# Optimization experiments

Measured on AMD Instinct MI355X. Metric: run time of the kernel, lower is better.

## Reference

```python
import jax, jax.numpy as jnp
import numpy as np

N = 100000   # nodes
E = 1600000  # edges per edge list (avg degree 16)
G = 512      # graphs in batch
D = 128      # hidden dim
BN_EPS = 1e-5


def setup_inputs() -> dict:
    key = jax.random.key(0)
    kit = iter(jax.random.split(key, 100))
    def nrm(shape, s=0.05):
        return jax.random.normal(next(kit), shape, dtype=jnp.float32) * s
    d = {}
    d['x_type'] = nrm((N, 3), 1.0)
    d['first'] = nrm((N, 13), 1.0)
    d['second'] = nrm((N, 13), 1.0)
    d['edge_attr'] = nrm((N, 4), 1.0)
    d['dist'] = jax.random.uniform(next(kit), (N, 1), dtype=jnp.float32)
    # encoder / fusion MLP blocks: Linear-BN-ReLU-Linear-BN-ReLU
    for pre, ind in (('te', 3), ('na', 26), ('ee', 5), ('m0', 3 * D)):
        d[pre + '_W1'] = nrm((ind, D)); d[pre + '_b1'] = jnp.zeros((D,), jnp.float32)
        d[pre + '_g1'] = jnp.ones((D,), jnp.float32); d[pre + '_be1'] = jnp.zeros((D,), jnp.float32)
        d[pre + '_W2'] = nrm((D, D)); d[pre + '_b2'] = jnp.zeros((D,), jnp.float32)
        d[pre + '_g2'] = jnp.ones((D,), jnp.float32); d[pre + '_be2'] = jnp.zeros((D,), jnp.float32)
    # 24 GINConv inner MLPs, stacked: layer L, conv k -> index 4*L+k (k: 1_l,2_l,1_g,2_g)
    d['gW1'] = nrm((24, D, D)); d['gb1'] = jnp.zeros((24, D), jnp.float32)
    d['gg1'] = jnp.ones((24, D), jnp.float32); d['gbe1'] = jnp.zeros((24, D), jnp.float32)
    d['gW2'] = nrm((24, D, D)); d['gb2'] = jnp.zeros((24, D), jnp.float32)
    d['gg2'] = jnp.ones((24, D), jnp.float32); d['gbe2'] = jnp.zeros((24, D), jnp.float32)
    d['geps'] = jnp.zeros((24,), jnp.float32)
    # 6 per-layer fusion MLPs (4*dim -> dim), stacked
    d['mW1'] = nrm((6, 4 * D, D)); d['mb1'] = jnp.zeros((6, D), jnp.float32)
    d['mg1'] = jnp.ones((6, D), jnp.float32); d['mbe1'] = jnp.zeros((6, D), jnp.float32)
    d['mW2'] = nrm((6, D, D)); d['mb2'] = jnp.zeros((6, D), jnp.float32)
    d['mg2'] = jnp.ones((6, D), jnp.float32); d['mbe2'] = jnp.zeros((6, D), jnp.float32)
    # Set2Set LSTM (input 2D, hidden D), torch gate order i,f,g,o
    d['Wih'] = nrm((4 * D, 2 * D)); d['Whh'] = nrm((4 * D, D))
    d['bih'] = jnp.zeros((4 * D,), jnp.float32); d['bhh'] = jnp.zeros((4 * D,), jnp.float32)
    d['fc1_W'] = nrm((2 * D, D)); d['fc1_b'] = jnp.zeros((D,), jnp.float32)
    d['fc4_W'] = nrm((D, 12)); d['fc4_b'] = jnp.zeros((12,), jnp.float32)
    for nm in ('ei_1l', 'ei_2l', 'ei_1g', 'ei_2g'):
        d[nm] = jax.random.randint(next(kit), (2, E), 0, N)
    d['batch'] = jnp.sort(jax.random.randint(next(kit), (N,), 0, G))
    return d


def _bn(h, g, b):
    # BatchNorm1d training-mode forward: biased batch stats
    m = h.mean(0)
    v = ((h - m) ** 2).mean(0)
    return g * (h - m) * jax.lax.rsqrt(v + BN_EPS) + b


def _block(h, W1, b1, g1, be1, W2, b2, g2, be2):
    h = jax.nn.relu(_bn(h @ W1 + b1, g1, be1))
    return jax.nn.relu(_bn(h @ W2 + b2, g2, be2))


def _forward(x_type, first, second, edge_attr, dist,
             te_W1, te_b1, te_g1, te_be1, te_W2, te_b2, te_g2, te_be2,
             na_W1, na_b1, na_g1, na_be1, na_W2, na_b2, na_g2, na_be2,
             ee_W1, ee_b1, ee_g1, ee_be1, ee_W2, ee_b2, ee_g2, ee_be2,
             m0_W1, m0_b1, m0_g1, m0_be1, m0_W2, m0_b2, m0_g2, m0_be2,
             gW1, gb1, gg1, gbe1, gW2, gb2, gg2, gbe2, geps,
             mW1, mb1, mg1, mbe1, mW2, mb2, mg2, mbe2,
             Wih, Whh, bih, bhh, fc1_W, fc1_b, fc4_W, fc4_b,
             ei_1l, ei_2l, ei_1g, ei_2g, batch):
    nl = _block(x_type, te_W1, te_b1, te_g1, te_be1, te_W2, te_b2, te_g2, te_be2)
    na = _block(jnp.concatenate([first, second], -1),
                na_W1, na_b1, na_g1, na_be1, na_W2, na_b2, na_g2, na_be2)
    ea = _block(jnp.concatenate([edge_attr, dist], -1),
                ee_W1, ee_b1, ee_g1, ee_be1, ee_W2, ee_b2, ee_g2, ee_be2)
    x = _block(jnp.concatenate([nl, na, ea], -1),
               m0_W1, m0_b1, m0_g1, m0_be1, m0_W2, m0_b2, m0_g2, m0_be2)

    def gin(h, ei, i):
        # GINConv: nn((1+eps)*x_i + sum_{j in N(i)} x_j); messages src=ei[0] -> dst=ei[1]
        agg = jnp.zeros_like(h).at[ei[1]].add(h[ei[0]])
        z = (1.0 + geps[i]) * h + agg
        return jax.nn.relu(_block(z, gW1[i], gb1[i], gg1[i], gbe1[i],
                                  gW2[i], gb2[i], gg2[i], gbe2[i]))

    for L in range(6):
        x1 = gin(x, ei_1l, 4 * L + 0)
        x2 = gin(x, ei_2l, 4 * L + 1)
        x3 = gin(x, ei_1g, 4 * L + 2)
        x4 = gin(x, ei_2g, 4 * L + 3)
        x = _block(jnp.concatenate([x1, x3, x2, x4], -1),
                   mW1[L], mb1[L], mg1[L], mbe1[L], mW2[L], mb2[L], mg2[L], mbe2[L])

    # Set2Set, 6 processing steps
    q_star = jnp.zeros((G, 2 * D), x.dtype)
    h = jnp.zeros((G, D), x.dtype)
    c = jnp.zeros((G, D), x.dtype)
    for _ in range(6):
        z = q_star @ Wih.T + h @ Whh.T + bih + bhh
        i_, f_, g_, o_ = jnp.split(z, 4, axis=1)
        c = jax.nn.sigmoid(f_) * c + jax.nn.sigmoid(i_) * jnp.tanh(g_)
        h = jax.nn.sigmoid(o_) * jnp.tanh(c)
        e = jnp.sum(x * h[batch], axis=-1)                     # [N]
        emax = jax.ops.segment_max(e, batch, num_segments=G)
        w = jnp.exp(e - emax[batch])
        den = jax.ops.segment_sum(w, batch, num_segments=G)
        a = w / den[batch]                                     # per-graph softmax
        r = jax.ops.segment_sum(a[:, None] * x, batch, num_segments=G)
        q_star = jnp.concatenate([h, r], axis=1)

    out = jax.nn.relu(q_star @ fc1_W + fc1_b) @ fc4_W + fc4_b  # [G, 12]
    return out


def reference(x_type, first, second, edge_attr, dist,
              te_W1, te_b1, te_g1, te_be1, te_W2, te_b2, te_g2, te_be2,
              na_W1, na_b1, na_g1, na_be1, na_W2, na_b2, na_g2, na_be2,
              ee_W1, ee_b1, ee_g1, ee_be1, ee_W2, ee_b2, ee_g2, ee_be2,
              m0_W1, m0_b1, m0_g1, m0_be1, m0_W2, m0_b2, m0_g2, m0_be2,
              gW1, gb1, gg1, gbe1, gW2, gb2, gg2, gbe2, geps,
              mW1, mb1, mg1, mbe1, mW2, mb2, mg2, mbe2,
              Wih, Whh, bih, bhh, fc1_W, fc1_b, fc4_W, fc4_b,
              ei_1l, ei_2l, ei_1g, ei_2g, batch):
    return _forward(x_type, first, second, edge_attr, dist,
                    te_W1, te_b1, te_g1, te_be1, te_W2, te_b2, te_g2, te_be2,
                    na_W1, na_b1, na_g1, na_be1, na_W2, na_b2, na_g2, na_be2,
                    ee_W1, ee_b1, ee_g1, ee_be1, ee_W2, ee_b2, ee_g2, ee_be2,
                    m0_W1, m0_b1, m0_g1, m0_be1, m0_W2, m0_b2, m0_g2, m0_be2,
                    gW1, gb1, gg1, gbe1, gW2, gb2, gg2, gbe2, geps,
                    mW1, mb1, mg1, mbe1, mW2, mb2, mg2, mbe2,
                    Wih, Whh, bih, bhh, fc1_W, fc1_b, fc4_W, fc4_b,
                    ei_1l, ei_2l, ei_1g, ei_2g, batch)
```

## Files before the change

kernel.cpp:

```cpp
#include <hip/hip_runtime.h>
#include <math.h>


#define DEV_INLINE __device__ __forceinline__
typedef unsigned short u16;

union F16U { _Float16 h; u16 u; };
DEV_INLINE float h2f(u16 v){ F16U t; t.u = v; return (float)t.h; }
DEV_INLINE u16 f2h(float f){ F16U t; t.h = (_Float16)f; return t.u; }
DEV_INLINE float bf2f(u16 h){ return __uint_as_float(((unsigned)h)<<16); }
DEV_INLINE u16 f2bf(float f){
  unsigned u = __float_as_uint(f);
  unsigned r = (u + 0x7FFFu + ((u>>16)&1u)) >> 16;
  return (u16)r;
}
DEV_INLINE float sigmoidf_(float x){ return 1.0f/(1.0f+expf(-x)); }
struct __align__(4) us2 { u16 x, y; };
struct __align__(8) us4 { u16 x, y, z, w; };

typedef __attribute__((ext_vector_type(8))) short s8v;
typedef __attribute__((ext_vector_type(4))) float f4v;

DEV_INLINE void bnsplit1(float f, u16& hb, u16& lb){
  hb = f2bf(f); lb = f2bf(f - bf2f(hb));
}

__global__ void zero_k(float* __restrict__ p, int n){
  int i = blockIdx.x*256 + threadIdx.x;
  if (i < n) p[i] = 0.f;
}

__global__ __launch_bounds__(256) void split_transpose(
  const float* __restrict__ src, u16* __restrict__ dh, u16* __restrict__ dl,
  int K, int count)
{
  int tot = count*K*128;
  for (int i = blockIdx.x*256 + threadIdx.x; i < tot; i += gridDim.x*256){
    int k = i % K;
    int n = (i / K) & 127;
    int c = i / (K*128);
    float w = src[(size_t)c*K*128 + (size_t)k*128 + n];
    u16 hi = f2bf(w);
    u16 lo = f2bf(w - bf2f(hi));
    dh[i] = hi; dl[i] = lo;
  }
}

__global__ void count_deg(const int* __restrict__ dst, int* __restrict__ cnt, int E){
  int e = blockIdx.x*256 + threadIdx.x;
  if (e < E) atomicAdd(&cnt[dst[e]], 1);
}

__global__ void scan_excl(const int* __restrict__ cnt, int* __restrict__ offs, int N){
  const int* c = cnt + (size_t)blockIdx.x * N;
  int* o = offs + (size_t)blockIdx.x * (N+1);
  __shared__ int ps[1024];
  int t = threadIdx.x;
  int chunk = (N + 1023) >> 10;
  int lo = t*chunk, hi = min(lo+chunk, N);
  int s = 0;
  for (int i=lo;i<hi;++i) s += c[i];
  ps[t] = s; __syncthreads();
  for (int d=1; d<1024; d<<=1){
    int v = (t>=d) ? ps[t-d] : 0;
    __syncthreads();
    ps[t] += v;
    __syncthreads();
  }
  int pre = (t==0) ? 0 : ps[t-1];
  for (int i=lo;i<hi;++i){ o[i]=pre; pre += c[i]; }
  if (t==1023) o[N] = ps[1023];
}

__global__ void fill_csr(const int* __restrict__ src, const int* __restrict__ dst,
                         const int* __restrict__ offs, int* __restrict__ cur,
                         int* __restrict__ out, int E){
  int e = blockIdx.x*256 + threadIdx.x;
  if (e >= E) return;
  int d = dst[e];
  int pos = offs[d] + atomicAdd(&cur[d], 1);
  out[pos] = src[e];
}

__global__ void sort_csr(const int* __restrict__ offs, int* __restrict__ srcs, int N){
  int i = blockIdx.x*256 + threadIdx.x;
  if (i >= N) return;
  int lo = offs[i], hi = offs[i+1];
  for (int a = lo+1; a < hi; ++a){
    int v = srcs[a];
    int b = a-1;
    while (b >= lo && srcs[b] > v){ srcs[b+1] = srcs[b]; --b; }
    srcs[b+1] = v;
  }
}

__global__ void graph_offsets(const int* __restrict__ batch, int* __restrict__ goff, int N, int G){
  int g = blockIdx.x*blockDim.x + threadIdx.x;
  if (g > G) return;
  int lo=0, hi=N;
  while (lo<hi){ int mid=(lo+hi)>>1; if (batch[mid] < g) lo=mid+1; else hi=mid; }
  goff[g]=lo;
}

__global__ __launch_bounds__(256) void stats_reduce1(
  const float* __restrict__ pstats, int PB, float* __restrict__ out2, int nb)
{
  int c = threadIdx.x, grp = blockIdx.x, bank = blockIdx.y;
  int chunk = (nb + 31) >> 5;
  int b0 = grp*chunk, b1 = min(b0+chunk, nb);
  const float* base = pstats + (size_t)bank*PB*256;
  float s = 0.f;
  for (int b=b0; b<b1; ++b) s += base[(size_t)b*256 + c];
  out2[((size_t)bank*32 + grp)*256 + c] = s;
}
__global__ __launch_bounds__(256) void bnfin2(
  const float* __restrict__ out2, const float* __restrict__ g,
  const float* __restrict__ be, float* __restrict__ Sb, float invN)
{
  __shared__ float tot[256];
  int t = threadIdx.x, bank = blockIdx.x;
  const float* src = out2 + (size_t)bank*32*256;
  float s = 0.f;
  #pragma unroll
  for (int j=0;j<32;++j) s += src[j*256 + t];
  tot[t] = s; __syncthreads();
  if (t < 128){
    float m = tot[t]*invN;
    float v = tot[128+t]*invN - m*m;
    float sc = g[bank*128 + t]*rsqrtf(v + 1e-5f);
    Sb[bank*256 + t] = sc;
    Sb[bank*256 + 128 + t] = be[bank*128 + t] - m*sc;
  }
}

#define GEMM_KS_BODY_F(A_, S_, WHp_, WLp_, Kel_)                              \
  {                                                                           \
    float4 sa0, sa1, sb0, sb1;                                                \
    if (S_){                                                                  \
      sa0 = *(const float4*)(S_ + koff);                                      \
      sa1 = *(const float4*)(S_ + koff + 4);                                  \
      sb0 = *(const float4*)(S_ + 128 + koff);                                \
      sb1 = *(const float4*)(S_ + 128 + koff + 4);                            \
    }                                                                         \
    s8v xh0, xl0, xh1, xl1;                                                   \
    _Pragma("unroll")                                                         \
    for (int mt=0; mt<2; ++mt){                                               \
      int row = wrow0 + mt*16 + m16;                                          \
      s8v xr = (row < N) ? *(const s8v*)(A_ + (size_t)row*128 + koff)         \
                         : (s8v){0,0,0,0,0,0,0,0};                            \
      float f0 = h2f((u16)xr[0]), f1 = h2f((u16)xr[1]);                       \
      float f2 = h2f((u16)xr[2]), f3 = h2f((u16)xr[3]);                       \
      float f4 = h2f((u16)xr[4]), f5 = h2f((u16)xr[5]);                       \
      float f6 = h2f((u16)xr[6]), f7 = h2f((u16)xr[7]);                       \
      if (S_){                                                                \
        f0 = fmaxf(fmaf(f0, sa0.x, sb0.x), 0.f);                              \
        f1 = fmaxf(fmaf(f1, sa0.y, sb0.y), 0.f);                              \
        f2 = fmaxf(fmaf(f2, sa0.z, sb0.z), 0.f);                              \
        f3 = fmaxf(fmaf(f3, sa0.w, sb0.w), 0.f);                              \
        f4 = fmaxf(fmaf(f4, sa1.x, sb1.x), 0.f);                              \
        f5 = fmaxf(fmaf(f5, sa1.y, sb1.y), 0.f);                              \
        f6 = fmaxf(fmaf(f6, sa1.z, sb1.z), 0.f);                              \
        f7 = fmaxf(fmaf(f7, sa1.w, sb1.w), 0.f);                              \
      }                                                                       \
      s8v h, l; u16 hb, lb;                                                   \
      bnsplit1(f0,hb,lb); h[0]=(short)hb; l[0]=(short)lb;                     \
      bnsplit1(f1,hb,lb); h[1]=(short)hb; l[1]=(short)lb;                     \
      bnsplit1(f2,hb,lb); h[2]=(short)hb; l[2]=(short)lb;                     \
      bnsplit1(f3,hb,lb); h[3]=(short)hb; l[3]=(short)lb;                     \
      bnsplit1(f4,hb,lb); h[4]=(short)hb; l[4]=(short)lb;                     \
      bnsplit1(f5,hb,lb); h[5]=(short)hb; l[5]=(short)lb;                     \
      bnsplit1(f6,hb,lb); h[6]=(short)hb; l[6]=(short)lb;                     \
      bnsplit1(f7,hb,lb); h[7]=(short)hb; l[7]=(short)lb;                     \
      if (mt==0){ xh0=h; xl0=l; } else { xh1=h; xl1=l; }                      \
    }                                                                         \
    _Pragma("unroll")                                                         \
    for (int nh=0; nh<2; ++nh){                                               \
      _Pragma("unroll")                                                       \
      for (int n4=0;n4<4;++n4){                                               \
        int n = (nh*4+n4)*16 + m16;                                           \
        size_t wa = (size_t)n*Kel_ + koff;                                    \
        s8v wh = *(const s8v*)(WHp_ + wa);                                    \
        s8v wl = *(const s8v*)(WLp_ + wa);                                    \
        acc[0][nh*4+n4] = __builtin_amdgcn_mfma_f32_16x16x32_bf16(wh, xh0, acc[0][nh*4+n4], 0,0,0); \
        acc[0][nh*4+n4] = __builtin_amdgcn_mfma_f32_16x16x32_bf16(wl, xh0, acc[0][nh*4+n4], 0,0,0); \
        acc[0][nh*4+n4] = __builtin_amdgcn_mfma_f32_16x16x32_bf16(wh, xl0, acc[0][nh*4+n4], 0,0,0); \
        acc[1][nh*4+n4] = __builtin_amdgcn_mfma_f32_16x16x32_bf16(wh, xh1, acc[1][nh*4+n4], 0,0,0); \
        acc[1][nh*4+n4] = __builtin_amdgcn_mfma_f32_16x16x32_bf16(wl, xh1, acc[1][nh*4+n4], 0,0,0); \
        acc[1][nh*4+n4] = __builtin_amdgcn_mfma_f32_16x16x32_bf16(wh, xl1, acc[1][nh*4+n4], 0,0,0); \
      }                                                                       \
    }                                                                         \
  }

#define GEMM_EPILOGUE_F(C_, bias_, pslot_)                                    \
  {                                                                           \
    _Pragma("unroll")                                                         \
    for (int nt=0;nt<8;++nt){                                                 \
      int n0 = nt*16 + kg*4;                                                  \
      float4 b4 = *(const float4*)(bias_ + n0);                               \
      float s1a=0.f,s1b=0.f,s1c=0.f,s1d=0.f;                                  \
      float s2a=0.f,s2b=0.f,s2c=0.f,s2d=0.f;                                  \
      _Pragma("unroll")                                                       \
      for (int mt=0;mt<2;++mt){                                               \
        int row = wrow0 + mt*16 + m16;                                        \
        us4 o;                                                                \
        o.x = f2h(acc[mt][nt][0] + b4.x);                                     \
        o.y = f2h(acc[mt][nt][1] + b4.y);                                     \
        o.z = f2h(acc[mt][nt][2] + b4.z);                                     \
        o.w = f2h(acc[mt][nt][3] + b4.w);                                     \
        *(us4*)(&cst[wid][mt][m16*136 + n0]) = o;                             \
        if (row < N){                                                         \
          float r0=h2f(o.x), r1=h2f(o.y), r2=h2f(o.z), r3=h2f(o.w);           \
          s1a+=r0; s1b+=r1; s1c+=r2; s1d+=r3;                                 \
          s2a+=r0*r0; s2b+=r1*r1; s2c+=r2*r2; s2d+=r3*r3;                     \
        }                                                                     \
      }                                                                       \
      _Pragma("unroll")                                                       \
      for (int off=1; off<16; off<<=1){                                       \
        s1a += __shfl_xor(s1a, off, 64); s1b += __shfl_xor(s1b, off, 64);     \
        s1c += __shfl_xor(s1c, off, 64); s1d += __shfl_xor(s1d, off, 64);     \
        s2a += __shfl_xor(s2a, off, 64); s2b += __shfl_xor(s2b, off, 64);     \
        s2c += __shfl_xor(s2c, off, 64); s2d += __shfl_xor(s2d, off, 64);     \
      }                                                                       \
      if (m16 == 0){                                                          \
        pw[wid][n0+0] = s1a; pw[wid][n0+1] = s1b;                             \
        pw[wid][n0+2] = s1c; pw[wid][n0+3] = s1d;                             \
        pw[wid][128+n0+0] = s2a; pw[wid][128+n0+1] = s2b;                     \
        pw[wid][128+n0+2] = s2c; pw[wid][128+n0+3] = s2d;                     \
      }                                                                       \
    }                                                                         \
    __syncthreads();                                                          \
    if (t < 256){                                                             \
      float tot = ((pw[0][t] + pw[1][t]) + pw[2][t]) + pw[3][t];              \
      (pslot_)[t] = tot;                                                      \
    }                                                                         \
    _Pragma("unroll")                                                         \
    for (int mt=0;mt<2;++mt){                                                 \
      _Pragma("unroll")                                                       \
      for (int it=0; it<4; ++it){                                             \
        int idx = it*64 + lane;                                               \
        int r = idx >> 4;                                                     \
        int c8 = (idx & 15) * 8;                                              \
        int row = wrow0 + mt*16 + r;                                          \
        if (row < N){                                                         \
          s8v v = *(const s8v*)(&cst[wid][mt][r*136 + c8]);                   \
          *(s8v*)(C_ + (size_t)row*128 + c8) = v;                             \
        }                                                                     \
      }                                                                       \
    }                                                                         \
  }

#define GEMM_KS_BODY_S(A_, S_, WHp_, WLp_, Kel_)                              \
  {                                                                           \
    float4 sa0, sa1, sb0, sb1;                                                \
    if (S_){                                                                  \
      sa0 = *(const float4*)(S_ + koff);                                      \
      sa1 = *(const float4*)(S_ + koff + 4);                                  \
      sb0 = *(const float4*)(S_ + 128 + koff);                                \
      sb1 = *(const float4*)(S_ + 128 + koff + 4);                            \
    }                                                                         \
    s8v xh0, xl0, xh1, xl1;                                                   \
    _Pragma("unroll")                                                         \
    for (int mt=0; mt<2; ++mt){                                               \
      int row = wrow0 + mt*16 + m16;                                          \
      s8v xr = (row < N) ? *(const s8v*)(A_ + (size_t)row*128 + koff)         \
                         : (s8v){0,0,0,0,0,0,0,0};                            \
      float f0 = h2f((u16)xr[0]), f1 = h2f((u16)xr[1]);                       \
      float f2 = h2f((u16)xr[2]), f3 = h2f((u16)xr[3]);                       \
      float f4 = h2f((u16)xr[4]), f5 = h2f((u16)xr[5]);                       \
      float f6 = h2f((u16)xr[6]), f7 = h2f((u16)xr[7]);                       \
      if (S_){                                                                \
        f0 = fmaxf(fmaf(f0, sa0.x, sb0.x), 0.f);                              \
        f1 = fmaxf(fmaf(f1, sa0.y, sb0.y), 0.f);                              \
        f2 = fmaxf(fmaf(f2, sa0.z, sb0.z), 0.f);                              \
        f3 = fmaxf(fmaf(f3, sa0.w, sb0.w), 0.f);                              \
        f4 = fmaxf(fmaf(f4, sa1.x, sb1.x), 0.f);                              \
        f5 = fmaxf(fmaf(f5, sa1.y, sb1.y), 0.f);                              \
        f6 = fmaxf(fmaf(f6, sa1.z, sb1.z), 0.f);                              \
        f7 = fmaxf(fmaf(f7, sa1.w, sb1.w), 0.f);                              \
      }                                                                       \
      s8v h, l; u16 hb, lb;                                                   \
      bnsplit1(f0,hb,lb); h[0]=(short)hb; l[0]=(short)lb;                     \
      bnsplit1(f1,hb,lb); h[1]=(short)hb; l[1]=(short)lb;                     \
      bnsplit1(f2,hb,lb); h[2]=(short)hb; l[2]=(short)lb;                     \
      bnsplit1(f3,hb,lb); h[3]=(short)hb; l[3]=(short)lb;                     \
      bnsplit1(f4,hb,lb); h[4]=(short)hb; l[4]=(short)lb;                     \
      bnsplit1(f5,hb,lb); h[5]=(short)hb; l[5]=(short)lb;                     \
      bnsplit1(f6,hb,lb); h[6]=(short)hb; l[6]=(short)lb;                     \
      bnsplit1(f7,hb,lb); h[7]=(short)hb; l[7]=(short)lb;                     \
      if (mt==0){ xh0=h; xl0=l; } else { xh1=h; xl1=l; }                      \
    }                                                                         \
    _Pragma("unroll")                                                         \
    for (int nt=0; nt<4; ++nt){                                               \
      int n = colbase + nt*16 + m16;                                          \
      size_t wa = (size_t)n*Kel_ + koff;                                      \
      s8v wh = *(const s8v*)(WHp_ + wa);                                      \
      s8v wl = *(const s8v*)(WLp_ + wa);                                      \
      acc[0][nt] = __builtin_amdgcn_mfma_f32_16x16x32_bf16(wh, xh0, acc[0][nt], 0,0,0); \
      acc[0][nt] = __builtin_amdgcn_mfma_f32_16x16x32_bf16(wl, xh0, acc[0][nt], 0,0,0); \
      acc[0][nt] = __builtin_amdgcn_mfma_f32_16x16x32_bf16(wh, xl0, acc[0][nt], 0,0,0); \
      acc[1][nt] = __builtin_amdgcn_mfma_f32_16x16x32_bf16(wh, xh1, acc[1][nt], 0,0,0); \
      acc[1][nt] = __builtin_amdgcn_mfma_f32_16x16x32_bf16(wl, xh1, acc[1][nt], 0,0,0); \
      acc[1][nt] = __builtin_amdgcn_mfma_f32_16x16x32_bf16(wh, xl1, acc[1][nt], 0,0,0); \
    }                                                                         \
  }

#define GEMM_EPILOGUE_S(C_, bias_, pslot_)                                    \
  {                                                                           \
    _Pragma("unroll")                                                         \
    for (int nt=0;nt<4;++nt){                                                 \
      int lc0 = nt*16 + kg*4;                                                 \
      int n0 = colbase + lc0;                                                 \
      float4 b4 = *(const float4*)(bias_ + n0);                               \
      float s1a=0.f,s1b=0.f,s1c=0.f,s1d=0.f;                                  \
      float s2a=0.f,s2b=0.f,s2c=0.f,s2d=0.f;                                  \
      _Pragma("unroll")                                                       \
      for (int mt=0;mt<2;++mt){                                               \
        int row = wrow0 + mt*16 + m16;                                        \
        us4 o;                                                                \
        o.x = f2h(acc[mt][nt][0] + b4.x);                                     \
        o.y = f2h(acc[mt][nt][1] + b4.y);                                     \
        o.z = f2h(acc[mt][nt][2] + b4.z);                                     \
        o.w = f2h(acc[mt][nt][3] + b4.w);                                     \
        *(us4*)(&cst[wid][mt][m16*72 + lc0]) = o;                             \
        if (row < N){                                                         \
          float r0=h2f(o.x), r1=h2f(o.y), r2=h2f(o.z), r3=h2f(o.w);           \
          s1a+=r0; s1b+=r1; s1c+=r2; s1d+=r3;                                 \
          s2a+=r0*r0; s2b+=r1*r1; s2c+=r2*r2; s2d+=r3*r3;                     \
        }                                                                     \
      }                                                                       \
      _Pragma("unroll")                                                       \
      for (int off=1; off<16; off<<=1){                                       \
        s1a += __shfl_xor(s1a, off, 64); s1b += __shfl_xor(s1b, off, 64);     \
        s1c += __shfl_xor(s1c, off, 64); s1d += __shfl_xor(s1d, off, 64);     \
        s2a += __shfl_xor(s2a, off, 64); s2b += __shfl_xor(s2b, off, 64);     \
        s2c += __shfl_xor(s2c, off, 64); s2d += __shfl_xor(s2d, off, 64);     \
      }                                                                       \
      if (m16 == 0){                                                          \
        pw[wid][lc0+0] = s1a; pw[wid][lc0+1] = s1b;                           \
        pw[wid][lc0+2] = s1c; pw[wid][lc0+3] = s1d;                           \
        pw[wid][64+lc0+0] = s2a; pw[wid][64+lc0+1] = s2b;                     \
        pw[wid][64+lc0+2] = s2c; pw[wid][64+lc0+3] = s2d;                     \
      }                                                                       \
    }                                                                         \
    __syncthreads();                                                          \
    if (t < 128){                                                             \
      int lc = t & 63, part = t >> 6;                                         \
      int li = part*64 + lc;                                                  \
      float tot = ((pw[0][li] + pw[1][li]) + pw[2][li]) + pw[3][li];          \
      (pslot_)[part*128 + colbase + lc] = tot;                                \
    }                                                                         \
    _Pragma("unroll")                                                         \
    for (int mt=0;mt<2;++mt){                                                 \
      _Pragma("unroll")                                                       \
      for (int it=0; it<2; ++it){                                             \
        int idx = it*64 + lane;                                               \
        int r = idx >> 3;                                                     \
        int c8 = (idx & 7) * 8;                                               \
        int row = wrow0 + mt*16 + r;                                          \
        if (row < N){                                                         \
          s8v v = *(const s8v*)(&cst[wid][mt][r*72 + c8]);                    \
          *(s8v*)(C_ + (size_t)row*128 + colbase + c8) = v;                   \
        }                                                                     \
      }                                                                       \
    }                                                                         \
  }

__global__ __launch_bounds__(256, 3) void gemm_rs_full(
  const u16* __restrict__ A0, const u16* __restrict__ A1,
  const u16* __restrict__ A2, const u16* __restrict__ A3,
  const float* __restrict__ S0, const float* __restrict__ S1,
  const float* __restrict__ S2, const float* __restrict__ S3,
  const u16* __restrict__ wt_hi, const u16* __restrict__ wt_lo,
  const float* __restrict__ bias,
  u16* __restrict__ C, float* __restrict__ pstats,
  int N, int npart)
{
  __shared__ u16 cst[4][2][16*136];
  __shared__ float pw[4][256];
  const int t = threadIdx.x;
  const int lane = t & 63;
  const int wid = t >> 6;
  const int m16 = lane & 15;
  const int kg = lane >> 4;
  const int wrow0 = blockIdx.x*128 + wid*32;
  const int K = npart << 7;

  f4v acc[2][8];
  #pragma unroll
  for (int i=0;i<2;++i)
    #pragma unroll
    for (int j=0;j<8;++j) acc[i][j] = (f4v){0.f,0.f,0.f,0.f};

  for (int part=0; part<npart; ++part){
    const u16* A = (part==0)?A0:(part==1)?A1:(part==2)?A2:A3;
    const float* S = (part==0)?S0:(part==1)?S1:(part==2)?S2:S3;
    const u16* WHp = wt_hi + part*128;
    const u16* WLp = wt_lo + part*128;
    #pragma unroll
    for (int ks=0; ks<4; ++ks){
      int koff = ks*32 + kg*8;
      GEMM_KS_BODY_F(A, S, WHp, WLp, K)
    }
  }
  GEMM_EPILOGUE_F(C, bias, (pstats + (size_t)blockIdx.x*256))
}

__global__ __launch_bounds__(256, 3) void gemm_rs_split(
  const u16* __restrict__ A0, const u16* __restrict__ A1,
  const u16* __restrict__ A2, const u16* __restrict__ A3,
  const float* __restrict__ S0, const float* __restrict__ S1,
  const float* __restrict__ S2, const float* __restrict__ S3,
  const u16* __restrict__ wt_hi, const u16* __restrict__ wt_lo,
  const float* __restrict__ bias,
  u16* __restrict__ C, float* __restrict__ pstats,
  int N, int npart)
{
  __shared__ u16 cst[4][2][16*72];
  __shared__ float pw[4][128];
  const int t = threadIdx.x;
  const int lane = t & 63;
  const int wid = t >> 6;
  const int m16 = lane & 15;
  const int kg = lane >> 4;
  const int wrow0 = blockIdx.x*128 + wid*32;
  const int colbase = blockIdx.y*64;
  const int K = npart << 7;

  f4v acc[2][4];
  #pragma unroll
  for (int i=0;i<2;++i)
    #pragma unroll
    for (int j=0;j<4;++j) acc[i][j] = (f4v){0.f,0.f,0.f,0.f};

  for (int part=0; part<npart; ++part){
    const u16* A = (part==0)?A0:(part==1)?A1:(part==2)?A2:A3;
    const float* S = (part==0)?S0:(part==1)?S1:(part==2)?S2:S3;
    const u16* WHp = wt_hi + part*128;
    const u16* WLp = wt_lo + part*128;
    #pragma unroll
    for (int ks=0; ks<4; ++ks){
      int koff = ks*32 + kg*8;
      GEMM_KS_BODY_S(A, S, WHp, WLp, K)
    }
  }
  GEMM_EPILOGUE_S(C, bias, (pstats + (size_t)blockIdx.x*256))
}

__global__ __launch_bounds__(256, 3) void gemm_gin(
  u16* __restrict__ Z0, u16* __restrict__ Z1,
  u16* __restrict__ Z2, u16* __restrict__ Z3,
  const float* __restrict__ Sbase,
  const u16* __restrict__ wt_hi, const u16* __restrict__ wt_lo,
  const float* __restrict__ bias,
  float* __restrict__ pstats, int PB,
  int N)
{
  __shared__ u16 cst[4][2][16*136];
  __shared__ float pw[4][256];
  const int t = threadIdx.x;
  const int lane = t & 63;
  const int wid = t >> 6;
  const int m16 = lane & 15;
  const int kg = lane >> 4;
  const int wrow0 = blockIdx.x*128 + wid*32;
  const int kb = blockIdx.y;

  u16* Zc = (kb==0)?Z0:(kb==1)?Z1:(kb==2)?Z2:Z3;
  const float* S = Sbase ? (Sbase + (size_t)kb*256) : nullptr;
  const u16* WHp = wt_hi + (size_t)kb*16384;
  const u16* WLp = wt_lo + (size_t)kb*16384;
  const float* biasp = bias + (size_t)kb*128;
  float* pslot = pstats + ((size_t)kb*PB + blockIdx.x)*256;

  f4v acc[2][8];
  #pragma unroll
  for (int i=0;i<2;++i)
    #pragma unroll
    for (int j=0;j<8;++j) acc[i][j] = (f4v){0.f,0.f,0.f,0.f};

  {
    const u16* A = Zc;
    #pragma unroll
    for (int ks=0; ks<4; ++ks){
      int koff = ks*32 + kg*8;
      GEMM_KS_BODY_F(A, S, WHp, WLp, 128)
    }
  }
  GEMM_EPILOGUE_F(Zc, biasp, pslot)
}

__global__ __launch_bounds__(256) void gemm_enc(
  const float* __restrict__ X0, int w0, const float* __restrict__ X1, int w1,
  const float* __restrict__ W, const float* __restrict__ bias,
  u16* __restrict__ C, float* __restrict__ pstats, int N)
{
  __shared__ float Ws[26*128];
  __shared__ float red[256];
  int K = w0 + w1;
  int t = threadIdx.x;
  for (int i=t;i<K*128;i+=256) Ws[i] = W[i];
  __syncthreads();
  int c = t & 127, rh = t >> 7;
  float b = bias[c];
  float s1=0.f, s2=0.f;
  for (int r0 = blockIdx.x*2; r0 < N; r0 += gridDim.x*2){
    int r = r0 + rh;
    if (r < N){
      float acc = b;
      for (int k=0;k<w0;++k) acc = fmaf(X0[(size_t)r*w0+k], Ws[k*128+c], acc);
      for (int k=0;k<w1;++k) acc = fmaf(X1[(size_t)r*w1+k], Ws[(w0+k)*128+c], acc);
      u16 o = f2h(acc);
      C[(size_t)r*128+c] = o;
      float rv = h2f(o);
      s1 += rv; s2 += rv*rv;
    }
  }
  red[t] = s1; __syncthreads();
  float t1 = (t < 128) ? (red[t] + red[t+128]) : 0.f;
  __syncthreads();
  red[t] = s2; __syncthreads();
  float t2 = (t < 128) ? (red[t] + red[t+128]) : 0.f;
  if (t < 128){
    pstats[(size_t)blockIdx.x*256 + t] = t1;
    pstats[(size_t)blockIdx.x*256 + 128 + t] = t2;
  }
}

__global__ __launch_bounds__(256) void aggregate4(
  const u16* __restrict__ X, const float* __restrict__ S,
  const int* __restrict__ srcs4, const int* __restrict__ offs4,
  int E, int Np1, const float* __restrict__ geps, int gi0,
  u16* __restrict__ Z0, u16* __restrict__ Z1,
  u16* __restrict__ Z2, u16* __restrict__ Z3, int N)
{
  int kb = blockIdx.y;
  const int* srcs = srcs4 + (size_t)kb*E;
  const int* offs = offs4 + (size_t)kb*Np1;
  u16* Z = (kb==0)?Z0:(kb==1)?Z1:(kb==2)?Z2:Z3;
  int i = blockIdx.x*4 + (threadIdx.x>>6);
  int ln = threadIdx.x & 63;
  int c = ln*2;
  if (i >= N) return;
  float sca = S[c], sha = S[128+c];
  float scb = S[c+1], shb = S[128+c+1];
  float eps1 = 1.0f + geps[gi0 + kb];
  us2 x0 = *(const us2*)(X + (size_t)i*128 + c);
  float acca = eps1 * fmaxf(fmaf(h2f(x0.x), sca, sha), 0.f);
  float accb = eps1 * fmaxf(fmaf(h2f(x0.y), scb, shb), 0.f);
  int e0 = offs[i], e1 = offs[i+1];
  int e = e0;
  for (; e+8 <= e1; e += 8){
    int s0 = srcs[e],   s1 = srcs[e+1], s2 = srcs[e+2], s3 = srcs[e+3];
    int s4 = srcs[e+4], s5 = srcs[e+5], s6 = srcs[e+6], s7 = srcs[e+7];
    us2 v0 = *(const us2*)(X + (size_t)s0*128 + c);
    us2 v1 = *(const us2*)(X + (size_t)s1*128 + c);
    us2 v2 = *(const us2*)(X + (size_t)s2*128 + c);
    us2 v3 = *(const us2*)(X + (size_t)s3*128 + c);
    us2 v4 = *(const us2*)(X + (size_t)s4*128 + c);
    us2 v5 = *(const us2*)(X + (size_t)s5*128 + c);
    us2 v6 = *(const us2*)(X + (size_t)s6*128 + c);
    us2 v7 = *(const us2*)(X + (size_t)s7*128 + c);
    acca += fmaxf(fmaf(h2f(v0.x), sca, sha), 0.f);
    accb += fmaxf(fmaf(h2f(v0.y), scb, shb), 0.f);
    acca += fmaxf(fmaf(h2f(v1.x), sca, sha), 0.f);
    accb += fmaxf(fmaf(h2f(v1.y), scb, shb), 0.f);
    acca += fmaxf(fmaf(h2f(v2.x), sca, sha), 0.f);
    accb += fmaxf(fmaf(h2f(v2.y), scb, shb), 0.f);
    acca += fmaxf(fmaf(h2f(v3.x), sca, sha), 0.f);
    accb += fmaxf(fmaf(h2f(v3.y), scb, shb), 0.f);
    acca += fmaxf(fmaf(h2f(v4.x), sca, sha), 0.f);
    accb += fmaxf(fmaf(h2f(v4.y), scb, shb), 0.f);
    acca += fmaxf(fmaf(h2f(v5.x), sca, sha), 0.f);
    accb += fmaxf(fmaf(h2f(v5.y), scb, shb), 0.f);
    acca += fmaxf(fmaf(h2f(v6.x), sca, sha), 0.f);
    accb += fmaxf(fmaf(h2f(v6.y), scb, shb), 0.f);
    acca += fmaxf(fmaf(h2f(v7.x), sca, sha), 0.f);
    accb += fmaxf(fmaf(h2f(v7.y), scb, shb), 0.f);
  }
  for (; e+4 <= e1; e += 4){
    int s0 = srcs[e], s1 = srcs[e+1], s2 = srcs[e+2], s3 = srcs[e+3];
    us2 v0 = *(const us2*)(X + (size_t)s0*128 + c);
    us2 v1 = *(const us2*)(X + (size_t)s1*128 + c);
    us2 v2 = *(const us2*)(X + (size_t)s2*128 + c);
    us2 v3 = *(const us2*)(X + (size_t)s3*128 + c);
    acca += fmaxf(fmaf(h2f(v0.x), sca, sha), 0.f);
    accb += fmaxf(fmaf(h2f(v0.y), scb, shb), 0.f);
    acca += fmaxf(fmaf(h2f(v1.x), sca, sha), 0.f);
    accb += fmaxf(fmaf(h2f(v1.y), scb, shb), 0.f);
    acca += fmaxf(fmaf(h2f(v2.x), sca, sha), 0.f);
    accb += fmaxf(fmaf(h2f(v2.y), scb, shb), 0.f);
    acca += fmaxf(fmaf(h2f(v3.x), sca, sha), 0.f);
    accb += fmaxf(fmaf(h2f(v3.y), scb, shb), 0.f);
  }
  for (; e < e1; ++e){
    int s = srcs[e];
    us2 xv = *(const us2*)(X + (size_t)s*128 + c);
    acca += fmaxf(fmaf(h2f(xv.x), sca, sha), 0.f);
    accb += fmaxf(fmaf(h2f(xv.y), scb, shb), 0.f);
  }
  us2 o; o.x = f2h(acca); o.y = f2h(accb);
  *(us2*)(Z + (size_t)i*128 + c) = o;
}

__global__ __launch_bounds__(256) void lstm_step(
  float* __restrict__ q_star, float* __restrict__ h, float* __restrict__ cst,
  const float* __restrict__ Wih, const float* __restrict__ Whh,
  const float* __restrict__ bih, const float* __restrict__ bhh, int G)
{
  __shared__ float q[256], hh[128], z[512];
  int t = threadIdx.x;
  for (int g = blockIdx.x; g < G; g += gridDim.x){
    q[t] = q_star[(size_t)g*256 + t];
    if (t < 128) hh[t] = h[(size_t)g*128 + t];
    __syncthreads();
    #pragma unroll
    for (int p=0;p<2;++p){
      int j = t + 256*p;
      float acc = bih[j] + bhh[j];
      const float* wi = Wih + (size_t)j*256;
      const float* wh = Whh + (size_t)j*128;
      for (int k=0;k<256;++k) acc = fmaf(q[k], wi[k], acc);
      for (int k=0;k<128;++k) acc = fmaf(hh[k], wh[k], acc);
      z[j] = acc;
    }
    __syncthreads();
    if (t < 128){
      float i_ = z[t], f_ = z[128+t], g_ = z[256+t], o_ = z[384+t];
      float cc = sigmoidf_(f_)*cst[(size_t)g*128+t] + sigmoidf_(i_)*tanhf(g_);
      float hn = sigmoidf_(o_)*tanhf(cc);
      cst[(size_t)g*128+t] = cc;
      h[(size_t)g*128+t]  = hn;
      q_star[(size_t)g*256+t] = hn;
    }
    __syncthreads();
  }
}

__global__ __launch_bounds__(256) void dot_h_hf(
  const u16* __restrict__ X, const float* __restrict__ S,
  const float* __restrict__ h, const int* __restrict__ batch,
  float* __restrict__ e, int N)
{
  int wv = threadIdx.x >> 6, ln = threadIdx.x & 63;
  int i = blockIdx.x*4 + wv;
  if (i >= N) return;
  int g = batch[i];
  int c = ln*2;
  us2 x2 = *(const us2*)(X + (size_t)i*128 + c);
  float2 h2 = *(const float2*)(h + (size_t)g*128 + c);
  float xa = fmaxf(fmaf(h2f(x2.x), S[c],   S[128+c]),   0.f);
  float xb = fmaxf(fmaf(h2f(x2.y), S[c+1], S[128+c+1]), 0.f);
  float p = xa*h2.x + xb*h2.y;
  #pragma unroll
  for (int off=32; off; off>>=1) p += __shfl_down(p, off, 64);
  if (ln==0) e[i] = p;
}

__global__ __launch_bounds__(256) void seg_reduce(
  const float* __restrict__ e, const int* __restrict__ goff,
  float* __restrict__ emax, float* __restrict__ invden, int G)
{
  int g = blockIdx.x;
  int lo = goff[g], hi = goff[g+1];
  int t = threadIdx.x;
  __shared__ float red[256];
  float m = -3.4e38f;
  for (int i=lo+t; i<hi; i+=256) m = fmaxf(m, e[i]);
  red[t] = m; __syncthreads();
  for (int d=128; d; d>>=1){ if (t<d) red[t] = fmaxf(red[t], red[t+d]); __syncthreads(); }
  m = red[0]; __syncthreads();
  float s = 0.f;
  for (int i=lo+t; i<hi; i+=256) s += expf(e[i]-m);
  red[t] = s; __syncthreads();
  for (int d=128; d; d>>=1){ if (t<d) red[t] += red[t+d]; __syncthreads(); }
  if (t==0){
    emax[g] = m;
    invden[g] = (hi>lo && red[0]>0.f) ? 1.f/red[0] : 0.f;
  }
}

__global__ __launch_bounds__(128) void r_kernel_hf(
  const u16* __restrict__ X, const float* __restrict__ S,
  const float* __restrict__ e, const int* __restrict__ goff,
  const float* __restrict__ emax, const float* __restrict__ invden,
  float* __restrict__ q_star, int G)
{
  int g = blockIdx.x, c = threadIdx.x;
  int lo = goff[g], hi = goff[g+1];
  float m = emax[g], inv = invden[g];
  float sc = S[c], sh = S[128+c];
  float r = 0.f;
  for (int i=lo; i<hi; ++i){
    float w = expf(e[i]-m);
    r = fmaf(w, fmaxf(fmaf(h2f(X[(size_t)i*128+c]), sc, sh), 0.f), r);
  }
  q_star[(size_t)g*256 + 128 + c] = r*inv;
}

__global__ __launch_bounds__(128) void final_k(
  const float* __restrict__ q_star, const float* __restrict__ fc1W,
  const float* __restrict__ fc1b, const float* __restrict__ fc4W,
  const float* __restrict__ fc4b, float* __restrict__ out, int G)
{
  __shared__ float q[256];
  __shared__ float h1[128];
  int g = blockIdx.x, t = threadIdx.x;
  q[t]     = q_star[(size_t)g*256 + t];
  q[128+t] = q_star[(size_t)g*256 + 128 + t];
  __syncthreads();
  float acc = fc1b[t];
  for (int k=0;k<256;++k) acc = fmaf(q[k], fc1W[(size_t)k*128+t], acc);
  h1[t] = fmaxf(acc, 0.f);
  __syncthreads();
  if (t < 12){
    float o = fc4b[t];
    for (int d=0; d<128; ++d) o = fmaf(h1[d], fc4W[(size_t)d*12+t], o);
    out[(size_t)g*12+t] = o;
  }
}

extern "C" void kernel_launch(void* const* d_in, const int* in_sizes, int n_in,
                              void* d_out, int out_size, void* d_ws, size_t ws_size,
                              hipStream_t stream)
{
  (void)n_in; (void)ws_size;
  const int N = in_sizes[0] / 3;
  const int E = in_sizes[62] / 2;
  const int G = out_size / 12;

  auto P = [&](int i){ return (const float*)d_in[i]; };
  const float* gb1 = P(38); const float* gg1 = P(39); const float* gbe1 = P(40);
  const float* gb2 = P(42); const float* gg2 = P(43); const float* gbe2 = P(44);
  const float* geps = P(45);
  const float* mb1 = P(47); const float* mg1 = P(48); const float* mbe1 = P(49);
  const float* mb2 = P(51); const float* mg2 = P(52); const float* mbe2 = P(53);
  const int* ei[4] = {(const int*)d_in[62], (const int*)d_in[63],
                      (const int*)d_in[64], (const int*)d_in[65]};
  const int* batch = (const int*)d_in[66];

  const int ggrid = (N + 127)/128;
  const int ENC_GRID = 1024;
  const int PB = (ggrid > ENC_GRID) ? ggrid : ENC_GRID;

  char* ws = (char*)d_ws;
  size_t off = 0;
  auto alloc = [&](size_t bytes)->char*{
    char* p = ws + off;
    off = (off + bytes + 255) & ~(size_t)255;
    return p;
  };
  u16* X = (u16*)alloc((size_t)N*128*2);
  u16* Z[4]; for (int k=0;k<4;++k) Z[k] = (u16*)alloc((size_t)N*128*2);
  float* ebuf  = (float*)alloc((size_t)N*4);
  float* pstats= (float*)alloc((size_t)4*PB*256*4);
  float* out2  = (float*)alloc((size_t)4*32*256*4);
  float* Sb    = (float*)alloc(9*256*4);
  int* offs4 = (int*)alloc((size_t)4*(N+1)*4);
  int* srcs4 = (int*)alloc((size_t)4*E*4);
  int* cnt4  = (int*)alloc((size_t)4*N*4);
  int* goff  = (int*)alloc((size_t)(G+1)*4);
  float* qstar = (float*)alloc((size_t)G*256*4);
  float* hbuf  = (float*)alloc((size_t)G*128*4);
  float* cbuf  = (float*)alloc((size_t)G*128*4);
  float* emax  = (float*)alloc((size_t)G*4);
  float* invden= (float*)alloc((size_t)G*4);
  const size_t WT_ELEMS = 1392640;
  u16* WTh = (u16*)alloc(WT_ELEMS*2);
  u16* WTl = (u16*)alloc(WT_ELEMS*2);

  const size_t oEnc0=0, oEnc1=16384, oEnc2=32768, oM0W1=49152, oM0W2=98304;
  const size_t oGW1=114688, oGW2=507904, oMW1=901120, oMW2=1294336;

  const float invN = 1.0f / (float)N;
  const int SX = 4, SZ0 = 5;
  auto Sl = [&](int i){ return Sb + (size_t)i*256; };

  auto prep = [&](const float* src, size_t o, int K, int count){
    int tot = count*K*128;
    split_transpose<<<(tot+255)/256,256,0,stream>>>(src, WTh+o, WTl+o, K, count);
  };
  prep(P(9),  oEnc0, 128, 1);
  prep(P(17), oEnc1, 128, 1);
  prep(P(25), oEnc2, 128, 1);
  prep(P(29), oM0W1, 384, 1);
  prep(P(33), oM0W2, 128, 1);
  prep(P(37), oGW1,  128, 24);
  prep(P(41), oGW2,  128, 24);
  prep(P(46), oMW1,  512, 6);
  prep(P(50), oMW2,  128, 6);

  int zgrid = (4*N + 255)/256;
  zero_k<<<zgrid,256,0,stream>>>((float*)cnt4, 4*N);
  int egrid = (E + 255)/256;
  for (int l=0;l<4;++l)
    count_deg<<<egrid,256,0,stream>>>(ei[l]+E, cnt4 + (size_t)l*N, E);
  scan_excl<<<4,1024,0,stream>>>(cnt4, offs4, N);
  zero_k<<<zgrid,256,0,stream>>>((float*)cnt4, 4*N);
  for (int l=0;l<4;++l)
    fill_csr<<<egrid,256,0,stream>>>(ei[l], ei[l]+E, offs4 + (size_t)l*(N+1),
                                     cnt4 + (size_t)l*N, srcs4 + (size_t)l*E, E);
  int ngrid = (N + 255)/256;
  for (int l=0;l<4;++l)
    sort_csr<<<ngrid,256,0,stream>>>(offs4 + (size_t)l*(N+1), srcs4 + (size_t)l*E, N);
  graph_offsets<<<(G+1+255)/256,256,0,stream>>>(batch, goff, N, G);

  auto run_bn = [&](int nbank, int nb, const float* g, const float* be, float* Sbase){
    stats_reduce1<<<dim3(32,nbank),256,0,stream>>>(pstats, PB, out2, nb);
    bnfin2<<<nbank,256,0,stream>>>(out2, g, be, Sbase, invN);
  };
  auto run_gemm_split = [&](const u16* A, const float* S, size_t wo, const float* b, u16* Cc){
    gemm_rs_split<<<dim3(ggrid,2),256,0,stream>>>(A,nullptr,nullptr,nullptr, S,nullptr,nullptr,nullptr,
                                                  WTh+wo, WTl+wo, b, Cc, pstats, N, 1);
  };
  auto run_gemm_full = [&](const u16* A, const float* S, size_t wo, const float* b, u16* Cc){
    gemm_rs_full<<<ggrid,256,0,stream>>>(A,nullptr,nullptr,nullptr, S,nullptr,nullptr,nullptr,
                                         WTh+wo, WTl+wo, b, Cc, pstats, N, 1);
  };

  gemm_enc<<<ENC_GRID,256,0,stream>>>(P(0),3, nullptr,0, P(5), P(6), X, pstats, N);
  run_bn(1, ENC_GRID, P(7), P(8), Sl(0));
  run_gemm_split(X, Sl(0), oEnc0, P(10), Z[0]);
  run_bn(1, ggrid, P(11), P(12), Sl(SZ0+0));

  gemm_enc<<<ENC_GRID,256,0,stream>>>(P(1),13, P(2),13, P(13), P(14), X, pstats, N);
  run_bn(1, ENC_GRID, P(15), P(16), Sl(0));
  run_gemm_split(X, Sl(0), oEnc1, P(18), Z[1]);
  run_bn(1, ggrid, P(19), P(20), Sl(SZ0+1));

  gemm_enc<<<ENC_GRID,256,0,stream>>>(P(3),4, P(4),1, P(21), P(22), X, pstats, N);
  run_bn(1, ENC_GRID, P(23), P(24), Sl(0));
  run_gemm_split(X, Sl(0), oEnc2, P(26), Z[2]);
  run_bn(1, ggrid, P(27), P(28), Sl(SZ0+2));

  gemm_rs_split<<<dim3(ggrid,2),256,0,stream>>>(Z[0],Z[1],Z[2],nullptr,
                                                Sl(SZ0+0),Sl(SZ0+1),Sl(SZ0+2),nullptr,
                                                WTh+oM0W1, WTl+oM0W1, P(30), X, pstats, N, 3);
  run_bn(1, ggrid, P(31), P(32), Sl(0));
  run_gemm_full(X, Sl(0), oM0W2, P(34), X);
  run_bn(1, ggrid, P(35), P(36), Sl(SX));

  int agrid = (N + 3)/4;
  for (int L=0; L<6; ++L){
    aggregate4<<<dim3(agrid,4),256,0,stream>>>(X, Sl(SX), srcs4, offs4, E, N+1,
                                               geps, 4*L, Z[0],Z[1],Z[2],Z[3], N);
    gemm_gin<<<dim3(ggrid,4),256,0,stream>>>(Z[0],Z[1],Z[2],Z[3], nullptr,
                                             WTh+oGW1+(size_t)4*L*16384,
                                             WTl+oGW1+(size_t)4*L*16384,
                                             gb1 + (size_t)4*L*128, pstats, PB, N);
    run_bn(4, ggrid, gg1 + (size_t)4*L*128, gbe1 + (size_t)4*L*128, Sl(0));
    gemm_gin<<<dim3(ggrid,4),256,0,stream>>>(Z[0],Z[1],Z[2],Z[3], Sl(0),
                                             WTh+oGW2+(size_t)4*L*16384,
                                             WTl+oGW2+(size_t)4*L*16384,
                                             gb2 + (size_t)4*L*128, pstats, PB, N);
    run_bn(4, ggrid, gg2 + (size_t)4*L*128, gbe2 + (size_t)4*L*128, Sl(SZ0));
    gemm_rs_split<<<dim3(ggrid,2),256,0,stream>>>(Z[0],Z[2],Z[1],Z[3],
                                                  Sl(SZ0+0),Sl(SZ0+2),Sl(SZ0+1),Sl(SZ0+3),
                                                  WTh+oMW1+(size_t)L*65536, WTl+oMW1+(size_t)L*65536,
                                                  mb1 + (size_t)L*128, X, pstats, N, 4);
    run_bn(1, ggrid, mg1 + (size_t)L*128, mbe1 + (size_t)L*128, Sl(0));
    run_gemm_full(X, Sl(0), oMW2 + (size_t)L*16384, mb2 + (size_t)L*128, X);
    run_bn(1, ggrid, mg2 + (size_t)L*128, mbe2 + (size_t)L*128, Sl(SX));
  }

  zero_k<<<(G*256+255)/256,256,0,stream>>>(qstar, G*256);
  zero_k<<<(G*128+255)/256,256,0,stream>>>(hbuf, G*128);
  zero_k<<<(G*128+255)/256,256,0,stream>>>(cbuf, G*128);
  int dgrid = (N + 3)/4;
  for (int s=0;s<6;++s){
    lstm_step<<<64,256,0,stream>>>(qstar, hbuf, cbuf, P(54), P(55), P(56), P(57), G);
    dot_h_hf<<<dgrid,256,0,stream>>>(X, Sl(SX), hbuf, batch, ebuf, N);
    seg_reduce<<<G,256,0,stream>>>(ebuf, goff, emax, invden, G);
    r_kernel_hf<<<G,128,0,stream>>>(X, Sl(SX), ebuf, goff, emax, invden, qstar, G);
  }

  final_k<<<G,128,0,stream>>>(qstar, P(58), P(59), P(60), P(61), (float*)d_out, G);
}
```

Baseline: 7.822 ms.

## Ping-pong activation buffers to use column-split GEMM; batch CSR build launches

```diff
diff --git a/kernel.cpp b/kernel.cpp
--- a/kernel.cpp
+++ b/kernel.cpp
@@ -46,9 +46,13 @@
   }
 }
 
-__global__ void count_deg(const int* __restrict__ dst, int* __restrict__ cnt, int E){
+__global__ void count_deg4(const int* __restrict__ e0, const int* __restrict__ e1,
+                           const int* __restrict__ e2, const int* __restrict__ e3,
+                           int* __restrict__ cnt, int E, int N){
+  int l = blockIdx.y;
+  const int* dst = ((l==0)?e0:(l==1)?e1:(l==2)?e2:e3) + E;
   int e = blockIdx.x*256 + threadIdx.x;
-  if (e < E) atomicAdd(&cnt[dst[e]], 1);
+  if (e < E) atomicAdd(&cnt[(size_t)l*N + dst[e]], 1);
 }
 
 __global__ void scan_excl(const int* __restrict__ cnt, int* __restrict__ offs, int N){
@@ -72,25 +76,34 @@
   if (t==1023) o[N] = ps[1023];
 }
 
-__global__ void fill_csr(const int* __restrict__ src, const int* __restrict__ dst,
-                         const int* __restrict__ offs, int* __restrict__ cur,
-                         int* __restrict__ out, int E){
+__global__ void fill_csr4(const int* __restrict__ e0, const int* __restrict__ e1,
+                          const int* __restrict__ e2, const int* __restrict__ e3,
+                          const int* __restrict__ offs4, int* __restrict__ cur,
+                          int* __restrict__ out, int E, int N){
+  int l = blockIdx.y;
+  const int* ei = (l==0)?e0:(l==1)?e1:(l==2)?e2:e3;
+  const int* src = ei;
+  const int* dst = ei + E;
   int e = blockIdx.x*256 + threadIdx.x;
   if (e >= E) return;
   int d = dst[e];
-  int pos = offs[d] + atomicAdd(&cur[d], 1);
-  out[pos] = src[e];
-}
-
-__global__ void sort_csr(const int* __restrict__ offs, int* __restrict__ srcs, int N){
+  int pos = offs4[(size_t)l*(N+1) + d] + atomicAdd(&cur[(size_t)l*N + d], 1);
+  out[(size_t)l*E + pos] = src[e];
+}
+
+__global__ void sort_csr4(const int* __restrict__ offs4, int* __restrict__ srcs,
+                          int E, int N){
+  int l = blockIdx.y;
   int i = blockIdx.x*256 + threadIdx.x;
   if (i >= N) return;
+  const int* offs = offs4 + (size_t)l*(N+1);
+  int* s = srcs + (size_t)l*E;
   int lo = offs[i], hi = offs[i+1];
   for (int a = lo+1; a < hi; ++a){
-    int v = srcs[a];
+    int v = s[a];
     int b = a-1;
-    while (b >= lo && srcs[b] > v){ srcs[b+1] = srcs[b]; --b; }
-    srcs[b+1] = v;
+    while (b >= lo && s[b] > v){ s[b+1] = s[b]; --b; }
+    s[b+1] = v;
   }
 }
 
@@ -364,46 +377,6 @@
       }                                                                       \
     }                                                                         \
   }
-
-__global__ __launch_bounds__(256, 3) void gemm_rs_full(
-  const u16* __restrict__ A0, const u16* __restrict__ A1,
-  const u16* __restrict__ A2, const u16* __restrict__ A3,
-  const float* __restrict__ S0, const float* __restrict__ S1,
-  const float* __restrict__ S2, const float* __restrict__ S3,
-  const u16* __restrict__ wt_hi, const u16* __restrict__ wt_lo,
-  const float* __restrict__ bias,
-  u16* __restrict__ C, float* __restrict__ pstats,
-  int N, int npart)
-{
-  __shared__ u16 cst[4][2][16*136];
-  __shared__ float pw[4][256];
-  const int t = threadIdx.x;
-  const int lane = t & 63;
-  const int wid = t >> 6;
-  const int m16 = lane & 15;
-  const int kg = lane >> 4;
-  const int wrow0 = blockIdx.x*128 + wid*32;
-  const int K = npart << 7;
-
-  f4v acc[2][8];
-  #pragma unroll
-  for (int i=0;i<2;++i)
-    #pragma unroll
-    for (int j=0;j<8;++j) acc[i][j] = (f4v){0.f,0.f,0.f,0.f};
-
-  for (int part=0; part<npart; ++part){
-    const u16* A = (part==0)?A0:(part==1)?A1:(part==2)?A2:A3;
-    const float* S = (part==0)?S0:(part==1)?S1:(part==2)?S2:S3;
-    const u16* WHp = wt_hi + part*128;
-    const u16* WLp = wt_lo + part*128;
-    #pragma unroll
-    for (int ks=0; ks<4; ++ks){
-      int koff = ks*32 + kg*8;
-      GEMM_KS_BODY_F(A, S, WHp, WLp, K)
-    }
-  }
-  GEMM_EPILOGUE_F(C, bias, (pstats + (size_t)blockIdx.x*256))
-}
 
 __global__ __launch_bounds__(256, 3) void gemm_rs_split(
   const u16* __restrict__ A0, const u16* __restrict__ A1,
@@ -749,8 +722,7 @@
     off = (off + bytes + 255) & ~(size_t)255;
     return p;
   };
-  u16* X = (u16*)alloc((size_t)N*128*2);
-  u16* Z[4]; for (int k=0;k<4;++k) Z[k] = (u16*)alloc((size_t)N*128*2);
+  u16* B[5]; for (int k=0;k<5;++k) B[k] = (u16*)alloc((size_t)N*128*2);
   float* ebuf  = (float*)alloc((size_t)N*4);
   float* pstats= (float*)alloc((size_t)4*PB*256*4);
   float* out2  = (float*)alloc((size_t)4*32*256*4);
@@ -775,6 +747,9 @@
   const int SX = 4, SZ0 = 5;
   auto Sl = [&](int i){ return Sb + (size_t)i*256; };
 
+  u16* xp = B[0];
+  u16* zp[4] = {B[1], B[2], B[3], B[4]};
+
   auto prep = [&](const float* src, size_t o, int K, int count){
     int tot = count*K*128;
     split_transpose<<<(tot+255)/256,256,0,stream>>>(src, WTh+o, WTl+o, K, count);
@@ -792,73 +767,67 @@
   int zgrid = (4*N + 255)/256;
   zero_k<<<zgrid,256,0,stream>>>((float*)cnt4, 4*N);
   int egrid = (E + 255)/256;
-  for (int l=0;l<4;++l)
-    count_deg<<<egrid,256,0,stream>>>(ei[l]+E, cnt4 + (size_t)l*N, E);
+  count_deg4<<<dim3(egrid,4),256,0,stream>>>(ei[0],ei[1],ei[2],ei[3], cnt4, E, N);
   scan_excl<<<4,1024,0,stream>>>(cnt4, offs4, N);
   zero_k<<<zgrid,256,0,stream>>>((float*)cnt4, 4*N);
-  for (int l=0;l<4;++l)
-    fill_csr<<<egrid,256,0,stream>>>(ei[l], ei[l]+E, offs4 + (size_t)l*(N+1),
-                                     cnt4 + (size_t)l*N, srcs4 + (size_t)l*E, E);
+  fill_csr4<<<dim3(egrid,4),256,0,stream>>>(ei[0],ei[1],ei[2],ei[3], offs4, cnt4, srcs4, E, N);
   int ngrid = (N + 255)/256;
-  for (int l=0;l<4;++l)
-    sort_csr<<<ngrid,256,0,stream>>>(offs4 + (size_t)l*(N+1), srcs4 + (size_t)l*E, N);
+  sort_csr4<<<dim3(ngrid,4),256,0,stream>>>(offs4, srcs4, E, N);
   graph_offsets<<<(G+1+255)/256,256,0,stream>>>(batch, goff, N, G);
 
   auto run_bn = [&](int nbank, int nb, const float* g, const float* be, float* Sbase){
     stats_reduce1<<<dim3(32,nbank),256,0,stream>>>(pstats, PB, out2, nb);
     bnfin2<<<nbank,256,0,stream>>>(out2, g, be, Sbase, invN);
   };
-  auto run_gemm_split = [&](const u16* A, const float* S, size_t wo, const float* b, u16* Cc){
+  auto run_gemm = [&](const u16* A, const float* S, size_t wo, const float* b, u16* Cc){
     gemm_rs_split<<<dim3(ggrid,2),256,0,stream>>>(A,nullptr,nullptr,nullptr, S,nullptr,nullptr,nullptr,
                                                   WTh+wo, WTl+wo, b, Cc, pstats, N, 1);
   };
-  auto run_gemm_full = [&](const u16* A, const float* S, size_t wo, const float* b, u16* Cc){
-    gemm_rs_full<<<ggrid,256,0,stream>>>(A,nullptr,nullptr,nullptr, S,nullptr,nullptr,nullptr,
-                                         WTh+wo, WTl+wo, b, Cc, pstats, N, 1);
-  };
-
-  gemm_enc<<<ENC_GRID,256,0,stream>>>(P(0),3, nullptr,0, P(5), P(6), X, pstats, N);
+
+  gemm_enc<<<ENC_GRID,256,0,stream>>>(P(0),3, nullptr,0, P(5), P(6), xp, pstats, N);
   run_bn(1, ENC_GRID, P(7), P(8), Sl(0));
-  run_gemm_split(X, Sl(0), oEnc0, P(10), Z[0]);
+  run_gemm(xp, Sl(0), oEnc0, P(10), zp[0]);
   run_bn(1, ggrid, P(11), P(12), Sl(SZ0+0));
 
-  gemm_enc<<<ENC_GRID,256,0,stream>>>(P(1),13, P(2),13, P(13), P(14), X, pstats, N);
+  gemm_enc<<<ENC_GRID,256,0,stream>>>(P(1),13, P(2),13, P(13), P(14), xp, pstats, N);
   run_bn(1, ENC_GRID, P(15), P(16), Sl(0));
-  run_gemm_split(X, Sl(0), oEnc1, P(18), Z[1]);
+  run_gemm(xp, Sl(0), oEnc1, P(18), zp[1]);
   run_bn(1, ggrid, P(19), P(20), Sl(SZ0+1));
 
-  gemm_enc<<<ENC_GRID,256,0,stream>>>(P(3),4, P(4),1, P(21), P(22), X, pstats, N);
+  gemm_enc<<<ENC_GRID,256,0,stream>>>(P(3),4, P(4),1, P(21), P(22), xp, pstats, N);
   run_bn(1, ENC_GRID, P(23), P(24), Sl(0));
-  run_gemm_split(X, Sl(0), oEnc2, P(26), Z[2]);
+  run_gemm(xp, Sl(0), oEnc2, P(26), zp[2]);
   run_bn(1, ggrid, P(27), P(28), Sl(SZ0+2));
 
-  gemm_rs_split<<<dim3(ggrid,2),256,0,stream>>>(Z[0],Z[1],Z[2],nullptr,
+  gemm_rs_split<<<dim3(ggrid,2),256,0,stream>>>(zp[0],zp[1],zp[2],nullptr,
                                                 Sl(SZ0+0),Sl(SZ0+1),Sl(SZ0+2),nullptr,
-                                                WTh+oM0W1, WTl+oM0W1, P(30), X, pstats, N, 3);
+                                                WTh+oM0W1, WTl+oM0W1, P(30), xp, pstats, N, 3);
   run_bn(1, ggrid, P(31), P(32), Sl(0));
-  run_gemm_full(X, Sl(0), oM0W2, P(34), X);
+  run_gemm(xp, Sl(0), oM0W2, P(34), zp[3]);
+  { u16* tmp = zp[3]; zp[3] = xp; xp = tmp; }
   run_bn(1, ggrid, P(35), P(36), Sl(SX));
 
   int agrid = (N + 3)/4;
   for (int L=0; L<6; ++L){
-    aggregate4<<<dim3(agrid,4),256,0,stream>>>(X, Sl(SX), srcs4, offs4, E, N+1,
-                                               geps, 4*L, Z[0],Z[1],Z[2],Z[3], N);
-    gemm_gin<<<dim3(ggrid,4),256,0,stream>>>(Z[0],Z[1],Z[2],Z[3], nullptr,
+    aggregate4<<<dim3(agrid,4),256,0,stream>>>(xp, Sl(SX), srcs4, offs4, E, N+1,
+                                               geps, 4*L, zp[0],zp[1],zp[2],zp[3], N);
+    gemm_gin<<<dim3(ggrid,4),256,0,stream>>>(zp[0],zp[1],zp[2],zp[3], nullptr,
                                              WTh+oGW1+(size_t)4*L*16384,
                                              WTl+oGW1+(size_t)4*L*16384,
                                              gb1 + (size_t)4*L*128, pstats, PB, N);
     run_bn(4, ggrid, gg1 + (size_t)4*L*128, gbe1 + (size_t)4*L*128, Sl(0));
-    gemm_gin<<<dim3(ggrid,4),256,0,stream>>>(Z[0],Z[1],Z[2],Z[3], Sl(0),
+    gemm_gin<<<dim3(ggrid,4),256,0,stream>>>(zp[0],zp[1],zp[2],zp[3], Sl(0),
                                              WTh+oGW2+(size_t)4*L*16384,
                                              WTl+oGW2+(size_t)4*L*16384,
                                              gb2 + (size_t)4*L*128, pstats, PB, N);
     run_bn(4, ggrid, gg2 + (size_t)4*L*128, gbe2 + (size_t)4*L*128, Sl(SZ0));
-    gemm_rs_split<<<dim3(ggrid,2),256,0,stream>>>(Z[0],Z[2],Z[1],Z[3],
+    gemm_rs_split<<<dim3(ggrid,2),256,0,stream>>>(zp[0],zp[2],zp[1],zp[3],
                                                   Sl(SZ0+0),Sl(SZ0+2),Sl(SZ0+1),Sl(SZ0+3),
                                                   WTh+oMW1+(size_t)L*65536, WTl+oMW1+(size_t)L*65536,
-                                                  mb1 + (size_t)L*128, X, pstats, N, 4);
+                                                  mb1 + (size_t)L*128, xp, pstats, N, 4);
     run_bn(1, ggrid, mg1 + (size_t)L*128, mbe1 + (size_t)L*128, Sl(0));
-    run_gemm_full(X, Sl(0), oMW2 + (size_t)L*16384, mb2 + (size_t)L*128, X);
+    run_gemm(xp, Sl(0), oMW2 + (size_t)L*16384, mb2 + (size_t)L*128, zp[0]);
+    { u16* tmp = zp[0]; zp[0] = xp; xp = tmp; }
     run_bn(1, ggrid, mg2 + (size_t)L*128, mbe2 + (size_t)L*128, Sl(SX));
   }
 
@@ -867,10 +836,10 @@
   zero_k<<<(G*128+255)/256,256,0,stream>>>(cbuf, G*128);
   int dgrid = (N + 3)/4;
   for (int s=0;s<6;++s){
-    lstm_step<<<64,256,0,stream>>>(qstar, hbuf, cbuf, P(54), P(55), P(56), P(57), G);
-    dot_h_hf<<<dgrid,256,0,stream>>>(X, Sl(SX), hbuf, batch, ebuf, N);
+    lstm_step<<<G,256,0,stream>>>(qstar, hbuf, cbuf, P(54), P(55), P(56), P(57), G);
+    dot_h_hf<<<dgrid,256,0,stream>>>(xp, Sl(SX), hbuf, batch, ebuf, N);
     seg_reduce<<<G,256,0,stream>>>(ebuf, goff, emax, invden, G);
-    r_kernel_hf<<<G,128,0,stream>>>(X, Sl(SX), ebuf, goff, emax, invden, qstar, G);
+    r_kernel_hf<<<G,128,0,stream>>>(xp, Sl(SX), ebuf, goff, emax, invden, qstar, G);
   }
 
   final_k<<<G,128,0,stream>>>(qstar, P(58), P(59), P(60), P(61), (float*)d_out, G);
```

After: 6.953 ms. -11.1%, faster.
